# Kernel optimization log

Hardware: AMD Instinct MI355X
Metric: run time of the kernel (lower is better)

## Reference

```python
import jax, jax.numpy as jnp
import numpy as np
import math

B, T, C, H = 4, 2048, 1024, 16
HD = C // H


def setup_inputs() -> dict:
    key = jax.random.key(0)
    ks = jax.random.split(key, 9)
    s = 1.0 / math.sqrt(C)
    return {
        "x": jax.random.normal(ks[0], (B, T, C), dtype=jnp.float32),
        "wq": jax.random.normal(ks[1], (C, C), dtype=jnp.float32) * s,
        "bq": jnp.zeros((C,), dtype=jnp.float32),
        "wk": jax.random.normal(ks[2], (C, C), dtype=jnp.float32) * s,
        "bk": jnp.zeros((C,), dtype=jnp.float32),
        "wv": jax.random.normal(ks[3], (C, C), dtype=jnp.float32) * s,
        "bv": jnp.zeros((C,), dtype=jnp.float32),
        "wp": jax.random.normal(ks[4], (C, C), dtype=jnp.float32) * s,
        "bp": jnp.zeros((C,), dtype=jnp.float32),
    }


def reference(x, wq, bq, wk, bk, wv, bv, wp, bp):
    b, t, c = x.shape
    # torch Linear: y = x @ W.T + b
    q = (x @ wq.T + bq).reshape(b, t, H, HD).transpose(0, 2, 1, 3)  # (B,H,T,hd)
    k = (x @ wk.T + bk).reshape(b, t, H, HD).transpose(0, 2, 1, 3)
    v = (x @ wv.T + bv).reshape(b, t, H, HD).transpose(0, 2, 1, 3)
    # NOTE: source scales by 1/sqrt(k.size(-1)) AFTER k.transpose(-2,-1),
    # i.e. 1/sqrt(T), not 1/sqrt(head_dim). Faithfully reproduced.
    scale = 1.0 / math.sqrt(t)
    scores = jnp.einsum("bhqd,bhkd->bhqk", q, k) * scale  # (B,H,T,T)
    causal = jnp.tril(jnp.ones((t, t), dtype=bool))
    scores = jnp.where(causal[None, None, :, :], scores, -jnp.inf)
    att = jax.nn.softmax(scores, axis=-1)
    out = jnp.einsum("bhqk,bhkd->bhqd", att, v)  # (B,H,T,hd)
    out = out.transpose(0, 2, 1, 3).reshape(b, t, c)
    return out @ wp.T + bp
```

## Files before the change

### kernel.cpp

```cpp
#include <hip/hip_runtime.h>
#include <hip/hip_bf16.h>
#include <stdint.h>
#include <math.h>

#define TB 2048
#define CD 1024

typedef short s16x8 __attribute__((ext_vector_type(8)));
typedef unsigned short u16x4 __attribute__((ext_vector_type(4)));
typedef float f32x4 __attribute__((ext_vector_type(4)));

#define QSCALE 0.02209708691207961f

__device__ __forceinline__ unsigned short f2bf(float f) {
    __hip_bfloat16 h = __float2bfloat16(f);
    return reinterpret_cast<unsigned short&>(h);
}

__device__ __forceinline__ void gl_lds16(const void* g, void* l) {
    typedef const __attribute__((address_space(1))) unsigned int gu32;
    typedef __attribute__((address_space(3))) unsigned int lu32;
    __builtin_amdgcn_global_load_lds((gu32*)g, (lu32*)l, 16, 0, 0);
}

__global__ void cast_k(const float* __restrict__ src, unsigned short* __restrict__ dst, int n4) {
    int i = blockIdx.x * blockDim.x + threadIdx.x;
    if (i < n4) {
        float4 v = reinterpret_cast<const float4*>(src)[i];
        u16x4 o = { f2bf(v.x), f2bf(v.y), f2bf(v.z), f2bf(v.w) };
        reinterpret_cast<u16x4*>(dst)[i] = o;
    }
}

template<int MODE>
__launch_bounds__(256)
__global__ void gemm_bt(const unsigned short* __restrict__ A,
                        const unsigned short* __restrict__ Bw,
                        unsigned short* __restrict__ qo,
                        unsigned short* __restrict__ ko,
                        unsigned short* __restrict__ vto,
                        const float* __restrict__ b0,
                        const float* __restrict__ b1,
                        const float* __restrict__ b2,
                        float* __restrict__ fout,
                        const float* __restrict__ bp)
{
    __shared__ unsigned short As[128 * 32];
    __shared__ unsigned short Bs[128 * 32];
    const int tid = threadIdx.x;
    const int mbase = blockIdx.y * 128;
    const int nbase = blockIdx.x * 128;
    const int lane = tid & 63;
    const int w = tid >> 6;
    const int g = lane >> 4;
    const int lr = lane & 15;
    const int wm = (w >> 1) * 64;
    const int wn = (w & 1) * 64;
    const int srow = lane >> 2;
    const int scol = (lane & 3) * 8;

    f32x4 acc[4][4];
#pragma unroll
    for (int i = 0; i < 4; ++i)
#pragma unroll
        for (int j = 0; j < 4; ++j) acc[i][j] = (f32x4)0.0f;

    const size_t arow0 = (size_t)(mbase + w * 16 + srow);
    const size_t arow1 = (size_t)(mbase + 64 + w * 16 + srow);
    const size_t brow0 = (size_t)(nbase + w * 16 + srow);
    const size_t brow1 = (size_t)(nbase + 64 + w * 16 + srow);
    unsigned short* asd0 = As + (w * 16) * 32;
    unsigned short* asd1 = As + (64 + w * 16) * 32;
    unsigned short* bsd0 = Bs + (w * 16) * 32;
    unsigned short* bsd1 = Bs + (64 + w * 16) * 32;

    for (int k0 = 0; k0 < 1024; k0 += 32) {
        __syncthreads();
        gl_lds16(A  + arow0 * 1024 + k0 + scol, asd0);
        gl_lds16(A  + arow1 * 1024 + k0 + scol, asd1);
        gl_lds16(Bw + brow0 * 1024 + k0 + scol, bsd0);
        gl_lds16(Bw + brow1 * 1024 + k0 + scol, bsd1);
        __syncthreads();
        s16x8 af[4], bfv[4];
#pragma unroll
        for (int mi = 0; mi < 4; ++mi)
            af[mi] = *reinterpret_cast<const s16x8*>(&As[(wm + mi * 16 + lr) * 32 + g * 8]);
#pragma unroll
        for (int ni = 0; ni < 4; ++ni)
            bfv[ni] = *reinterpret_cast<const s16x8*>(&Bs[(wn + ni * 16 + lr) * 32 + g * 8]);
#pragma unroll
        for (int mi = 0; mi < 4; ++mi)
#pragma unroll
            for (int ni = 0; ni < 4; ++ni)
                acc[mi][ni] = __builtin_amdgcn_mfma_f32_16x16x32_bf16(af[mi], bfv[ni], acc[mi][ni], 0, 0, 0);
    }

#pragma unroll
    for (int mi = 0; mi < 4; ++mi) {
        const int mg = mbase + wm + mi * 16 + g * 4;
#pragma unroll
        for (int ni = 0; ni < 4; ++ni) {
            const int ng = nbase + wn + ni * 16 + lr;
            if constexpr (MODE == 0) {
                const int which = ng >> 10;
                const int nin = ng & 1023;
                const float bias = (which == 0) ? b0[nin] : (which == 1) ? b1[nin] : b2[nin];
                const int h = nin >> 6, d = nin & 63;
                const int b = mg >> 11, t = mg & 2047;
                if (which == 2) {
                    u16x4 pv = { f2bf(acc[mi][ni][0] + bias), f2bf(acc[mi][ni][1] + bias),
                                 f2bf(acc[mi][ni][2] + bias), f2bf(acc[mi][ni][3] + bias) };
                    *reinterpret_cast<u16x4*>(vto + ((size_t)((b * 16 + h) * 64 + d)) * 2048 + t) = pv;
                } else if (which == 0) {
#pragma unroll
                    for (int r = 0; r < 4; ++r)
                        qo[((size_t)(b * 16 + h) * 2048 + (t + r)) * 64 + d] =
                            f2bf((acc[mi][ni][r] + bias) * QSCALE);
                } else {
#pragma unroll
                    for (int r = 0; r < 4; ++r)
                        ko[((size_t)(b * 16 + h) * 2048 + (t + r)) * 64 + d] = f2bf(acc[mi][ni][r] + bias);
                }
            } else {
                const float bias = bp[ng];
#pragma unroll
                for (int r = 0; r < 4; ++r)
                    fout[(size_t)(mg + r) * 1024 + ng] = acc[mi][ni][r] + bias;
            }
        }
    }
}

__launch_bounds__(512, 4)
__global__ void attn_k(const unsigned short* __restrict__ qg,
                       const unsigned short* __restrict__ kg,
                       const unsigned short* __restrict__ vtg,
                       unsigned short* __restrict__ og)
{
    __shared__ unsigned short Kt[2][64 * 64];
    __shared__ unsigned short Vs[2][64 * 64];
    __shared__ unsigned short P_lds[8][16 * 64];

    const int pr = blockIdx.x;
    const int bh = blockIdx.y;
    const int b = bh >> 4, h = bh & 15;
    const int tid = threadIdx.x;
    const int w = tid >> 6;
    const int lane = tid & 63;
    const int g = lane >> 4;
    const int lr = lane & 15;

    const unsigned short* Qp = qg + (size_t)bh * TB * 64;
    const unsigned short* Kp = kg + (size_t)bh * TB * 64;
    const unsigned short* Vt = vtg + (size_t)bh * 64 * TB;
    unsigned short* Pw = P_lds[w];

    const int srow = lane >> 3;
    const int schk = lane & 7;
    const int gchk = schk ^ srow;
    const int swz = lr & 7;

#pragma unroll 1
    for (int half = 0; half < 2; ++half) {
        const int sup = half == 0 ? pr : 15 - pr;
        const int qw = sup * 128 + w * 16;
        const int ntw = (qw >> 6) + 1;
        const int NT = sup * 2 + 2;

        const unsigned short* qp = Qp + (size_t)(qw + lr) * 64 + g * 8;
        s16x8 bq0 = *reinterpret_cast<const s16x8*>(qp);
        s16x8 bq1 = *reinterpret_cast<const s16x8*>(qp + 32);

        f32x4 oacc[4];
#pragma unroll
        for (int dt = 0; dt < 4; ++dt) oacc[dt] = (f32x4)0.0f;
        float mi_ = -INFINITY, li_ = 0.0f;

        asm volatile("s_waitcnt lgkmcnt(0)" ::: "memory");
        __builtin_amdgcn_s_barrier();
        gl_lds16(Kp + (size_t)(w * 8 + srow) * 64 + gchk * 8, &Kt[0][w * 512]);
        gl_lds16(Vt + (size_t)(w * 8 + srow) * TB + gchk * 8, &Vs[0][w * 512]);
        asm volatile("s_waitcnt vmcnt(0)" ::: "memory");
        __builtin_amdgcn_s_barrier();
        asm volatile("" ::: "memory");
        __builtin_amdgcn_sched_barrier(0);

        int cur = 0;
#pragma unroll 1
        for (int t = 0; t < NT; ++t) {
            const int other = cur ^ 1;
            if (t > 0) {
                asm volatile("s_waitcnt lgkmcnt(0)" ::: "memory");
                __builtin_amdgcn_s_barrier();
            }
            if (t + 1 < NT) {
                const int k0n = (t + 1) * 64;
                gl_lds16(Kp + (size_t)(k0n + w * 8 + srow) * 64 + gchk * 8, &Kt[other][w * 512]);
                gl_lds16(Vt + (size_t)(w * 8 + srow) * TB + k0n + gchk * 8, &Vs[other][w * 512]);
                asm volatile("s_waitcnt vmcnt(2)" ::: "memory");
            } else {
                asm volatile("s_waitcnt vmcnt(0)" ::: "memory");
            }
            __builtin_amdgcn_s_barrier();
            asm volatile("" ::: "memory");
            __builtin_amdgcn_sched_barrier(0);

            if (t < ntw) {
                const unsigned short* Kc = Kt[cur];
                const unsigned short* Vc = Vs[cur];
                f32x4 st[4];
#pragma unroll
                for (int sub = 0; sub < 4; ++sub) {
                    const unsigned short* krow = Kc + (sub * 16 + lr) * 64;
                    s16x8 ak0 = *reinterpret_cast<const s16x8*>(krow + ((g ^ swz) * 8));
                    s16x8 ak1 = *reinterpret_cast<const s16x8*>(krow + (((g + 4) ^ swz) * 8));
                    f32x4 z = (f32x4)0.0f;
                    z = __builtin_amdgcn_mfma_f32_16x16x32_bf16(ak0, bq0, z, 0, 0, 0);
                    st[sub] = __builtin_amdgcn_mfma_f32_16x16x32_bf16(ak1, bq1, z, 0, 0, 0);
                }
                if (t == ntw - 1) {
                    const int k0 = t * 64;
#pragma unroll
                    for (int sub = 0; sub < 4; ++sub)
#pragma unroll
                        for (int r = 0; r < 4; ++r) {
                            const int key = k0 + sub * 16 + g * 4 + r;
                            if (key > qw + lr) st[sub][r] = -INFINITY;
                        }
                }
                float mloc = st[0][0];
#pragma unroll
                for (int sub = 0; sub < 4; ++sub)
#pragma unroll
                    for (int r = 0; r < 4; ++r) mloc = fmaxf(mloc, st[sub][r]);
                mloc = fmaxf(mloc, __shfl_xor(mloc, 16));
                mloc = fmaxf(mloc, __shfl_xor(mloc, 32));
                if (__any(mloc - mi_ > 8.0f)) {
                    const float mn = fmaxf(mi_, mloc);
                    const float alpha = __expf(mi_ - mn);
                    li_ *= alpha;
#pragma unroll
                    for (int dt = 0; dt < 4; ++dt) oacc[dt] *= alpha;
                    mi_ = mn;
                }
                float ps = 0.0f;
#pragma unroll
                for (int sub = 0; sub < 4; ++sub)
#pragma unroll
                    for (int r = 0; r < 4; ++r) {
                        const float p = __expf(st[sub][r] - mi_);
                        st[sub][r] = p;
                        ps += p;
                    }
                ps += __shfl_xor(ps, 16);
                ps += __shfl_xor(ps, 32);
                li_ += ps;
#pragma unroll
                for (int sub = 0; sub < 4; ++sub) {
                    u16x4 pk = { f2bf(st[sub][0]), f2bf(st[sub][1]),
                                 f2bf(st[sub][2]), f2bf(st[sub][3]) };
                    const int bo = sub * 32 + g * 8;
                    const int phys = ((bo >> 4) ^ swz) * 16 + (bo & 15);
                    *reinterpret_cast<u16x4*>(reinterpret_cast<char*>(Pw + lr * 64) + phys) = pk;
                }
#pragma unroll
                for (int ks = 0; ks < 2; ++ks) {
                    const int gran = (ks * 4 + g) ^ swz;
                    s16x8 pb = *reinterpret_cast<const s16x8*>(
                        reinterpret_cast<const char*>(Pw + lr * 64) + gran * 16);
#pragma unroll
                    for (int dt = 0; dt < 4; ++dt) {
                        s16x8 vfr = *reinterpret_cast<const s16x8*>(
                            Vc + (dt * 16 + lr) * 64 + (((ks * 4 + g) ^ swz) * 8));
                        oacc[dt] = __builtin_amdgcn_mfma_f32_16x16x32_bf16(vfr, pb, oacc[dt], 0, 0, 0);
                    }
                }
            }
            cur = other;
        }

        const float inv_l = 1.0f / li_;
        unsigned short* orow = og + ((size_t)(b * TB + qw + lr)) * CD + h * 64;
#pragma unroll
        for (int dt = 0; dt < 4; ++dt) {
            u16x4 ov = { f2bf(oacc[dt][0] * inv_l), f2bf(oacc[dt][1] * inv_l),
                         f2bf(oacc[dt][2] * inv_l), f2bf(oacc[dt][3] * inv_l) };
            *reinterpret_cast<u16x4*>(orow + dt * 16 + g * 4) = ov;
        }
    }
}

extern "C" void kernel_launch(void* const* d_in, const int* in_sizes, int n_in,
                              void* d_out, int out_size, void* d_ws, size_t ws_size,
                              hipStream_t stream)
{
    const float* x  = (const float*)d_in[0];
    const float* wq = (const float*)d_in[1];
    const float* bq = (const float*)d_in[2];
    const float* wk = (const float*)d_in[3];
    const float* bk = (const float*)d_in[4];
    const float* wv = (const float*)d_in[5];
    const float* bv = (const float*)d_in[6];
    const float* wp = (const float*)d_in[7];
    const float* bp = (const float*)d_in[8];
    float* out = (float*)d_out;

    unsigned short* xb   = (unsigned short*)d_ws;
    unsigned short* wcat = xb + 8388608;
    unsigned short* wpb  = wcat + 3145728;
    unsigned short* qb_  = wpb + 1048576;
    unsigned short* kb_  = qb_ + 8388608;
    unsigned short* vtb  = kb_ + 8388608;
    unsigned short* ob   = xb;

    cast_k<<<8192, 256, 0, stream>>>(x, xb, 2097152);
    cast_k<<<1024, 256, 0, stream>>>(wq, wcat, 262144);
    cast_k<<<1024, 256, 0, stream>>>(wk, wcat + 1048576, 262144);
    cast_k<<<1024, 256, 0, stream>>>(wv, wcat + 2097152, 262144);
    cast_k<<<1024, 256, 0, stream>>>(wp, wpb, 262144);

    gemm_bt<0><<<dim3(24, 64), 256, 0, stream>>>(xb, wcat, qb_, kb_, vtb,
                                                 bq, bk, bv, nullptr, nullptr);
    attn_k<<<dim3(8, 64), 512, 0, stream>>>(qb_, kb_, vtb, ob);
    gemm_bt<1><<<dim3(8, 64), 256, 0, stream>>>(ob, wpb, nullptr, nullptr, nullptr,
                                                nullptr, nullptr, nullptr, out, bp);
}
```

Baseline: 274.8 us.

## Deepen GEMM K-tile to 64 with XOR-swizzled LDS; prioritize attention MFMA sections

The projection GEMM now stages a 64-wide K slice per iteration instead of 32. This halves the number of barrier pairs and load phases. LDS rows are XOR-swizzled by chunk so the wider rows avoid bank conflicts on fragment reads. In the attention kernel, s_setprio raises wave priority around the QK and PV MFMA blocks, and the row-max reduction becomes a tree. The cost is double the LDS per GEMM block, which may reduce occupancy.

```diff
diff --git a/kernel.cpp b/kernel.cpp
--- a/kernel.cpp
+++ b/kernel.cpp
@@ -45,8 +45,8 @@
                         float* __restrict__ fout,
                         const float* __restrict__ bp)
 {
-    __shared__ unsigned short As[128 * 32];
-    __shared__ unsigned short Bs[128 * 32];
+    __shared__ unsigned short As[128 * 64];
+    __shared__ unsigned short Bs[128 * 64];
     const int tid = threadIdx.x;
     const int mbase = blockIdx.y * 128;
     const int nbase = blockIdx.x * 128;
@@ -56,8 +56,8 @@
     const int lr = lane & 15;
     const int wm = (w >> 1) * 64;
     const int wn = (w & 1) * 64;
-    const int srow = lane >> 2;
-    const int scol = (lane & 3) * 8;
+    const int srow8 = lane >> 3;
+    const int gchk = (lane & 7) ^ srow8;
 
     f32x4 acc[4][4];
 #pragma unroll
@@ -65,34 +65,36 @@
 #pragma unroll
         for (int j = 0; j < 4; ++j) acc[i][j] = (f32x4)0.0f;
 
-    const size_t arow0 = (size_t)(mbase + w * 16 + srow);
-    const size_t arow1 = (size_t)(mbase + 64 + w * 16 + srow);
-    const size_t brow0 = (size_t)(nbase + w * 16 + srow);
-    const size_t brow1 = (size_t)(nbase + 64 + w * 16 + srow);
-    unsigned short* asd0 = As + (w * 16) * 32;
-    unsigned short* asd1 = As + (64 + w * 16) * 32;
-    unsigned short* bsd0 = Bs + (w * 16) * 32;
-    unsigned short* bsd1 = Bs + (64 + w * 16) * 32;
-
-    for (int k0 = 0; k0 < 1024; k0 += 32) {
+    const unsigned short* Arow = A  + (size_t)(mbase + w * 32 + srow8) * 1024 + gchk * 8;
+    const unsigned short* Brow = Bw + (size_t)(nbase + w * 32 + srow8) * 1024 + gchk * 8;
+    unsigned short* asd = As + (w * 32) * 64;
+    unsigned short* bsd = Bs + (w * 32) * 64;
+    const int xswz = lr & 7;
+
+    for (int k0 = 0; k0 < 1024; k0 += 64) {
         __syncthreads();
-        gl_lds16(A  + arow0 * 1024 + k0 + scol, asd0);
-        gl_lds16(A  + arow1 * 1024 + k0 + scol, asd1);
-        gl_lds16(Bw + brow0 * 1024 + k0 + scol, bsd0);
-        gl_lds16(Bw + brow1 * 1024 + k0 + scol, bsd1);
+#pragma unroll
+        for (int i = 0; i < 4; ++i) {
+            gl_lds16(Arow + (size_t)(i * 8) * 1024 + k0, asd + i * 8 * 64);
+            gl_lds16(Brow + (size_t)(i * 8) * 1024 + k0, bsd + i * 8 * 64);
+        }
         __syncthreads();
-        s16x8 af[4], bfv[4];
-#pragma unroll
-        for (int mi = 0; mi < 4; ++mi)
-            af[mi] = *reinterpret_cast<const s16x8*>(&As[(wm + mi * 16 + lr) * 32 + g * 8]);
-#pragma unroll
-        for (int ni = 0; ni < 4; ++ni)
-            bfv[ni] = *reinterpret_cast<const s16x8*>(&Bs[(wn + ni * 16 + lr) * 32 + g * 8]);
-#pragma unroll
-        for (int mi = 0; mi < 4; ++mi)
+#pragma unroll
+        for (int kk = 0; kk < 2; ++kk) {
+            const int xr = ((kk * 4 + g) ^ xswz) * 8;
+            s16x8 af[4], bfv[4];
+#pragma unroll
+            for (int mi = 0; mi < 4; ++mi)
+                af[mi] = *reinterpret_cast<const s16x8*>(&As[(wm + mi * 16 + lr) * 64 + xr]);
 #pragma unroll
             for (int ni = 0; ni < 4; ++ni)
-                acc[mi][ni] = __builtin_amdgcn_mfma_f32_16x16x32_bf16(af[mi], bfv[ni], acc[mi][ni], 0, 0, 0);
+                bfv[ni] = *reinterpret_cast<const s16x8*>(&Bs[(wn + ni * 16 + lr) * 64 + xr]);
+#pragma unroll
+            for (int mi = 0; mi < 4; ++mi)
+#pragma unroll
+                for (int ni = 0; ni < 4; ++ni)
+                    acc[mi][ni] = __builtin_amdgcn_mfma_f32_16x16x32_bf16(af[mi], bfv[ni], acc[mi][ni], 0, 0, 0);
+        }
     }
 
 #pragma unroll
@@ -153,11 +155,10 @@
     const unsigned short* Qp = qg + (size_t)bh * TB * 64;
     const unsigned short* Kp = kg + (size_t)bh * TB * 64;
     const unsigned short* Vt = vtg + (size_t)bh * 64 * TB;
-    unsigned short* Pw = P_lds[w];
+    char* prow = reinterpret_cast<char*>(&P_lds[w][lr * 64]);
 
     const int srow = lane >> 3;
-    const int schk = lane & 7;
-    const int gchk = schk ^ srow;
+    const int gchk = (lane & 7) ^ srow;
     const int swz = lr & 7;
 
 #pragma unroll 1
@@ -209,6 +210,7 @@
                 const unsigned short* Kc = Kt[cur];
                 const unsigned short* Vc = Vs[cur];
                 f32x4 st[4];
+                __builtin_amdgcn_s_setprio(1);
 #pragma unroll
                 for (int sub = 0; sub < 4; ++sub) {
                     const unsigned short* krow = Kc + (sub * 16 + lr) * 64;
@@ -218,6 +220,7 @@
                     z = __builtin_amdgcn_mfma_f32_16x16x32_bf16(ak0, bq0, z, 0, 0, 0);
                     st[sub] = __builtin_amdgcn_mfma_f32_16x16x32_bf16(ak1, bq1, z, 0, 0, 0);
                 }
+                __builtin_amdgcn_s_setprio(0);
                 if (t == ntw - 1) {
                     const int k0 = t * 64;
 #pragma unroll
@@ -228,11 +231,11 @@
                             if (key > qw + lr) st[sub][r] = -INFINITY;
                         }
                 }
-                float mloc = st[0][0];
-#pragma unroll
-                for (int sub = 0; sub < 4; ++sub)
-#pragma unroll
-                    for (int r = 0; r < 4; ++r) mloc = fmaxf(mloc, st[sub][r]);
+                float m0 = fmaxf(fmaxf(st[0][0], st[0][1]), fmaxf(st[0][2], st[0][3]));
+                float m1 = fmaxf(fmaxf(st[1][0], st[1][1]), fmaxf(st[1][2], st[1][3]));
+                float m2 = fmaxf(fmaxf(st[2][0], st[2][1]), fmaxf(st[2][2], st[2][3]));
+                float m3 = fmaxf(fmaxf(st[3][0], st[3][1]), fmaxf(st[3][2], st[3][3]));
+                float mloc = fmaxf(fmaxf(m0, m1), fmaxf(m2, m3));
                 mloc = fmaxf(mloc, __shfl_xor(mloc, 16));
                 mloc = fmaxf(mloc, __shfl_xor(mloc, 32));
                 if (__any(mloc - mi_ > 8.0f)) {
@@ -261,13 +264,13 @@
                                  f2bf(st[sub][2]), f2bf(st[sub][3]) };
                     const int bo = sub * 32 + g * 8;
                     const int phys = ((bo >> 4) ^ swz) * 16 + (bo & 15);
-                    *reinterpret_cast<u16x4*>(reinterpret_cast<char*>(Pw + lr * 64) + phys) = pk;
-                }
+                    *reinterpret_cast<u16x4*>(prow + phys) = pk;
+                }
+                __builtin_amdgcn_s_setprio(1);
 #pragma unroll
                 for (int ks = 0; ks < 2; ++ks) {
                     const int gran = (ks * 4 + g) ^ swz;
-                    s16x8 pb = *reinterpret_cast<const s16x8*>(
-                        reinterpret_cast<const char*>(Pw + lr * 64) + gran * 16);
+                    s16x8 pb = *reinterpret_cast<const s16x8*>(prow + gran * 16);
 #pragma unroll
                     for (int dt = 0; dt < 4; ++dt) {
                         s16x8 vfr = *reinterpret_cast<const s16x8*>(
@@ -275,6 +278,7 @@
                         oacc[dt] = __builtin_amdgcn_mfma_f32_16x16x32_bf16(vfr, pb, oacc[dt], 0, 0, 0);
                     }
                 }
+                __builtin_amdgcn_s_setprio(0);
             }
             cur = other;
         }
```

New measurement: 269.0 us. 1.02x faster.
